# Kernel optimization log

Measured on AMD Instinct MI355X. Metric: run time of the kernel, lower is better.

The kernel has to match this reference:

```python
import jax, jax.numpy as jnp
import numpy as np

MAX_X = 128
B, S, H, D = 2, 512, 8, 64
E = H * D  # embed_dim = 512


def setup_inputs() -> dict:
    key = jax.random.key(0)
    k1, k2, k3 = jax.random.split(key, 3)
    q = jax.random.normal(k1, (B, S, H, D), dtype=jnp.float32)
    embed_table = jax.random.normal(k2, (2 * MAX_X + 1, E), dtype=jnp.float32)
    x = jax.random.randint(k3, (B, S), 0, MAX_X, dtype=jnp.int64)
    return {"q": q, "embed_table": embed_table, "x": x, "max_x": MAX_X}


def reference(q, embed_table, x, max_x):
    # rel[b, i, j] = max_x + x[b, j] - x[b, i]  (faithful to x.reshape(-1,1,S) - x.reshape(-1,S,1))
    rel = max_x + x[:, None, :] - x[:, :, None]          # [B, S, S] int
    rel_e = embed_table[rel]                              # [B, S, S, E] gather
    b, s = rel.shape[0], rel.shape[1]
    h, d = q.shape[2], q.shape[3]
    rel_e = rel_e.reshape(b, s, s, h, d)                  # [B, Sq, Sk, H, D]
    # scores[b, h, q, k] = sum_d q[b, q, h, d] * rel_e[b, q, k, h, d]
    return jnp.einsum('bqhd,bqkhd->bhqk', q, rel_e)
```

## Files before the change

kernel.cpp:

```cpp
#include <hip/hip_runtime.h>


#define S_LEN 512
#define NH 8
#define HD 64
#define EDIM 512
#define TI 16

__global__ __launch_bounds__(256) void relpos_kernel(
    const float* __restrict__ q,
    const float* __restrict__ et,
    const int*   __restrict__ x,
    const int*   __restrict__ maxx_p,
    float*       __restrict__ out)
{
    const int tid = threadIdx.x;
    const int per = S_LEN / TI;
    const int b   = blockIdx.x / (NH * per);
    const int h   = (blockIdx.x / per) % NH;
    const int i0  = (blockIdx.x % per) * TI;

    __shared__ float q_lds[TI * HD];
    __shared__ float t_lds[TI][256];
    __shared__ int   xi_lds[TI];

    {
        const int ii = tid >> 4;
        const int k  = tid & 15;
        const float4 v = *(const float4*)(q + (((size_t)b * S_LEN + i0 + ii) * NH + h) * HD + k * 4);
        *(float4*)(q_lds + tid * 4) = v;
    }
    if (tid < TI) xi_lds[tid] = x[b * S_LEN + i0 + tid];

    const float4* trow = (const float4*)(et + (size_t)tid * EDIM + h * HD);
    float4 treg[16];
    #pragma unroll
    for (int k = 0; k < 16; ++k) treg[k] = trow[k];

    const int2 xj = *(const int2*)(x + b * S_LEN + 2 * tid);
    const int maxx = maxx_p[0];

    __syncthreads();

    float acc[TI];
    #pragma unroll
    for (int ii = 0; ii < TI; ++ii) acc[ii] = 0.f;

    #pragma unroll
    for (int k = 0; k < 16; ++k) {
        const float4 t4 = treg[k];
        #pragma unroll
        for (int ii = 0; ii < TI; ++ii) {
            const float4 q4 = *(const float4*)(q_lds + ii * HD + k * 4);
            acc[ii] += q4.x * t4.x + q4.y * t4.y + q4.z * t4.z + q4.w * t4.w;
        }
    }
    #pragma unroll
    for (int ii = 0; ii < TI; ++ii) t_lds[ii][tid] = acc[ii];

    __syncthreads();

    float* obase = out + (((size_t)b * NH + h) * S_LEN + i0) * S_LEN;
    #pragma unroll
    for (int ii = 0; ii < TI; ++ii) {
        const int xi = xi_lds[ii];
        const int r0 = (maxx + xj.x - xi) & 255;
        const int r1 = (maxx + xj.y - xi) & 255;
        float2 o;
        o.x = t_lds[ii][r0];
        o.y = t_lds[ii][r1];
        *(float2*)(obase + (size_t)ii * S_LEN + 2 * tid) = o;
    }
}

extern "C" void kernel_launch(void* const* d_in, const int* in_sizes, int n_in,
                              void* d_out, int out_size, void* d_ws, size_t ws_size,
                              hipStream_t stream) {
    const float* q    = (const float*)d_in[0];
    const float* et   = (const float*)d_in[1];
    const int*   x    = (const int*)d_in[2];
    const int*   maxx = (const int*)d_in[3];
    float*       out  = (float*)d_out;

    const int B = in_sizes[2] / S_LEN;
    dim3 grid(B * NH * (S_LEN / TI));
    relpos_kernel<<<grid, 256, 0, stream>>>(q, et, x, maxx, out);
}
```

Before: 75.62 us.

## Compute q-by-table dot products with bf16 MFMA instead of scalar FP32

Replaces the per-thread FP32 dot-product loop over 256 table rows with MFMA 16x16x32 bf16 instructions. The table slice and the q tile are converted to bf16 and staged in padded LDS. Results are scattered into padded shared memory before the same gather-and-store epilogue. This cuts ALU work and register pressure from holding 16 float4s per thread, but it lowers precision to bf16 inputs, which may exceed tolerance. The kernel is likely bound by the output writes, so the gain may be small.

Measured after the change: 67.52 us. -10.7%, faster.

```diff
diff --git a/kernel.cpp b/kernel.cpp
--- a/kernel.cpp
+++ b/kernel.cpp
@@ -6,6 +6,18 @@
 #define HD 64
 #define EDIM 512
 #define TI 16
+#define NR 256
+#define TPAD 72
+#define OPAD 257
+
+typedef __attribute__((ext_vector_type(8))) short bf16x8;
+typedef __attribute__((ext_vector_type(4))) float f32x4;
+
+__device__ __forceinline__ unsigned short f2bf(float f) {
+    union { float f; unsigned u; } v; v.f = f;
+    unsigned r = v.u + 0x7fffu + ((v.u >> 16) & 1u);
+    return (unsigned short)(r >> 16);
+}
 
 __global__ __launch_bounds__(256) void relpos_kernel(
     const float* __restrict__ q,
@@ -20,55 +32,74 @@
     const int h   = (blockIdx.x / per) % NH;
     const int i0  = (blockIdx.x % per) * TI;
 
-    __shared__ float q_lds[TI * HD];
-    __shared__ float t_lds[TI][256];
-    __shared__ int   xi_lds[TI];
+    __shared__ unsigned short Tl[NR][TPAD];
+    __shared__ unsigned short Ql[TI][TPAD];
+    __shared__ float          Ts[TI][OPAD];
+    __shared__ int            xi_s[TI];
 
+    const int row16 = tid >> 4;
+    const int k4    = tid & 15;
+
+    #pragma unroll
+    for (int p = 0; p < 16; ++p) {
+        const int r = p * 16 + row16;
+        const float4 v = *(const float4*)(et + (size_t)r * EDIM + h * HD + k4 * 4);
+        ushort4 u;
+        u.x = f2bf(v.x); u.y = f2bf(v.y); u.z = f2bf(v.z); u.w = f2bf(v.w);
+        *(ushort4*)&Tl[r][k4 * 4] = u;
+    }
     {
-        const int ii = tid >> 4;
-        const int k  = tid & 15;
-        const float4 v = *(const float4*)(q + (((size_t)b * S_LEN + i0 + ii) * NH + h) * HD + k * 4);
-        *(float4*)(q_lds + tid * 4) = v;
+        const float4 v = *(const float4*)(q + (((size_t)b * S_LEN + i0 + row16) * NH + h) * HD + k4 * 4);
+        ushort4 u;
+        u.x = f2bf(v.x); u.y = f2bf(v.y); u.z = f2bf(v.z); u.w = f2bf(v.w);
+        *(ushort4*)&Ql[row16][k4 * 4] = u;
     }
-    if (tid < TI) xi_lds[tid] = x[b * S_LEN + i0 + tid];
-
-    const float4* trow = (const float4*)(et + (size_t)tid * EDIM + h * HD);
-    float4 treg[16];
-    #pragma unroll
-    for (int k = 0; k < 16; ++k) treg[k] = trow[k];
-
+    if (tid < TI) xi_s[tid] = x[b * S_LEN + i0 + tid];
     const int2 xj = *(const int2*)(x + b * S_LEN + 2 * tid);
     const int maxx = maxx_p[0];
 
     __syncthreads();
 
-    float acc[TI];
+    const int w    = tid >> 6;
+    const int l    = tid & 63;
+    const int quad = l >> 4;
+    const int c    = l & 15;
+
+    const bf16x8 a0 = *(const bf16x8*)&Ql[c][quad * 8];
+    const bf16x8 a1 = *(const bf16x8*)&Ql[c][32 + quad * 8];
+
+    f32x4 acc[4];
     #pragma unroll
-    for (int ii = 0; ii < TI; ++ii) acc[ii] = 0.f;
+    for (int nt = 0; nt < 4; ++nt) acc[nt] = (f32x4){0.f, 0.f, 0.f, 0.f};
 
     #pragma unroll
-    for (int k = 0; k < 16; ++k) {
-        const float4 t4 = treg[k];
+    for (int nt = 0; nt < 4; ++nt) {
+        const int r = w * 64 + nt * 16 + c;
+        const bf16x8 b0 = *(const bf16x8*)&Tl[r][quad * 8];
+        const bf16x8 b1 = *(const bf16x8*)&Tl[r][32 + quad * 8];
+        acc[nt] = __builtin_amdgcn_mfma_f32_16x16x32_bf16(a0, b0, acc[nt], 0, 0, 0);
+        acc[nt] = __builtin_amdgcn_mfma_f32_16x16x32_bf16(a1, b1, acc[nt], 0, 0, 0);
+    }
+
+    #pragma unroll
+    for (int nt = 0; nt < 4; ++nt) {
         #pragma unroll
-        for (int ii = 0; ii < TI; ++ii) {
-            const float4 q4 = *(const float4*)(q_lds + ii * HD + k * 4);
-            acc[ii] += q4.x * t4.x + q4.y * t4.y + q4.z * t4.z + q4.w * t4.w;
+        for (int v = 0; v < 4; ++v) {
+            Ts[quad * 4 + v][w * 64 + nt * 16 + c] = acc[nt][v];
         }
     }
-    #pragma unroll
-    for (int ii = 0; ii < TI; ++ii) t_lds[ii][tid] = acc[ii];
 
     __syncthreads();
 
     float* obase = out + (((size_t)b * NH + h) * S_LEN + i0) * S_LEN;
     #pragma unroll
     for (int ii = 0; ii < TI; ++ii) {
-        const int xi = xi_lds[ii];
+        const int xi = xi_s[ii];
         const int r0 = (maxx + xj.x - xi) & 255;
         const int r1 = (maxx + xj.y - xi) & 255;
         float2 o;
-        o.x = t_lds[ii][r0];
-        o.y = t_lds[ii][r1];
+        o.x = Ts[ii][r0];
+        o.y = Ts[ii][r1];
         *(float2*)(obase + (size_t)ii * S_LEN + 2 * tid) = o;
     }
 }
```
